# Kernel tuning notes

Hardware: AMD Instinct MI355X
Metric: run time of the kernel (lower is better)

Reference implementation:

```python
import jax, jax.numpy as jnp
import numpy as np

N_EMB = 768
N_HEAD = 12
B, T = 2, 2048
LN_EPS = 1e-5


def _ln(x, g, b):
    mu = jnp.mean(x, axis=-1, keepdims=True)
    var = jnp.mean((x - mu) ** 2, axis=-1, keepdims=True)
    return (x - mu) * jax.lax.rsqrt(var + LN_EPS) * g + b


def setup_inputs() -> dict:
    key = jax.random.key(0)
    ks = jax.random.split(key, 12)
    s = 0.02
    d = {
        "x": jax.random.normal(ks[0], (B, T, N_EMB), dtype=jnp.float32),
        "cond_len": 256,
        "padding_mask": jax.random.randint(ks[1], (B, T), 0, 2, dtype=jnp.int32),
        "g1": jnp.ones((N_EMB,), jnp.float32),
        "bln1": jnp.zeros((N_EMB,), jnp.float32),
        "g2": jnp.ones((N_EMB,), jnp.float32),
        "bln2": jnp.zeros((N_EMB,), jnp.float32),
        "Wq": jax.random.normal(ks[2], (N_EMB, N_EMB), jnp.float32) * s,
        "bq": jnp.zeros((N_EMB,), jnp.float32),
        "Wk": jax.random.normal(ks[3], (N_EMB, N_EMB), jnp.float32) * s,
        "bk": jnp.zeros((N_EMB,), jnp.float32),
        "Wv": jax.random.normal(ks[4], (N_EMB, N_EMB), jnp.float32) * s,
        "bv": jnp.zeros((N_EMB,), jnp.float32),
        "Wp": jax.random.normal(ks[5], (N_EMB, N_EMB), jnp.float32) * s,
        "bp": jnp.zeros((N_EMB,), jnp.float32),
        "W1": jax.random.normal(ks[6], (4 * N_EMB, N_EMB), jnp.float32) * s,
        "b1": jnp.zeros((4 * N_EMB,), jnp.float32),
        "W2": jax.random.normal(ks[7], (N_EMB, 4 * N_EMB), jnp.float32) * s,
        "b2": jnp.zeros((N_EMB,), jnp.float32),
    }
    return d


def reference(x, cond_len, padding_mask, g1, bln1, g2, bln2,
              Wq, bq, Wk, bk, Wv, bv, Wp, bp, W1, b1, W2, b2):
    Bc, Tc, C = x.shape
    H = N_HEAD
    Dh = C // H
    h = _ln(x, g1, bln1)
    q = (h @ Wq.T + bq).reshape(Bc, Tc, H, Dh)
    k = (h @ Wk.T + bk).reshape(Bc, Tc, H, Dh)
    v = (h @ Wv.T + bv).reshape(Bc, Tc, H, Dh)
    att = jnp.einsum("bqhd,bkhd->bhqk", q, k) * (1.0 / np.sqrt(Dh))
    # mask: key col allowed if col >= cond_len OR col < n_b, n_b = T - sum(pmask_b)
    n = Tc - jnp.sum(padding_mask, axis=1)  # [B]
    cols = jnp.arange(Tc)
    allowed = (cols[None, :] >= cond_len) | (cols[None, :] < n[:, None])  # [B,T]
    att = jnp.where(allowed[:, None, None, :], att, -jnp.inf)
    att = jax.nn.softmax(att, axis=-1)
    y = jnp.einsum("bhqk,bkhd->bqhd", att, v).reshape(Bc, Tc, C)
    x = x + (y @ Wp.T + bp)
    h2 = _ln(x, g2, bln2)
    m = jax.nn.gelu(h2 @ W1.T + b1, approximate=False) @ W2.T + b2
    return x + m
```

## Files before the change

kernel.cpp:

```cpp
#include <hip/hip_runtime.h>
#include <hip/hip_bf16.h>
#include <math.h>

typedef short bf16x8 __attribute__((ext_vector_type(8)));
typedef float f32x4 __attribute__((ext_vector_type(4)));
typedef float f32x16 __attribute__((ext_vector_type(16)));
typedef unsigned short us4 __attribute__((ext_vector_type(4)));

#define MFMA16(a, b, c) __builtin_amdgcn_mfma_f32_16x16x32_bf16(a, b, c, 0, 0, 0)
#define MFMA32(a, b, c) __builtin_amdgcn_mfma_f32_32x32x16_bf16(a, b, c, 0, 0, 0)

__device__ __forceinline__ unsigned short f2b(float f) {
  unsigned int u = __builtin_bit_cast(unsigned int, f);
  u += 0x7fffu + ((u >> 16) & 1u);
  return (unsigned short)(u >> 16);
}

__device__ __forceinline__ float b2f(unsigned short u) {
  unsigned int x = ((unsigned int)u) << 16;
  return __builtin_bit_cast(float, x);
}

__device__ __forceinline__ unsigned int cvtpk(float lo, float hiv) {
  unsigned int r;
  asm("v_cvt_pk_bf16_f32 %0, %1, %2" : "=v"(r) : "v"(lo), "v"(hiv));
  return r;
}

__device__ __forceinline__ void gload16(const void* g, void* l) {
  __builtin_amdgcn_global_load_lds((const unsigned int*)g, (unsigned int*)l, 16, 0, 0);
}

__global__ void cvt_qkv_k(const float* __restrict__ wq, const float* __restrict__ wk,
                          const float* __restrict__ wv, unsigned short* __restrict__ dst) {
  int i = blockIdx.x * 256 + threadIdx.x;
  if (i >= 2304 * 768 / 4) return;
  int e = i * 4;
  const float* src = e < 589824 ? wq + e : (e < 1179648 ? wk + (e - 589824) : wv + (e - 1179648));
  float4 v = *(const float4*)src;
  us4 o; o.x = f2b(v.x); o.y = f2b(v.y); o.z = f2b(v.z); o.w = f2b(v.w);
  ((us4*)dst)[i] = o;
}

__global__ void cvt3_k(const float* __restrict__ s0, const float* __restrict__ s1,
                       const float* __restrict__ s2, unsigned short* __restrict__ d0,
                       unsigned short* __restrict__ d1, unsigned short* __restrict__ d2) {
  const int n0 = 147456, n1 = 589824, n2 = 589824;
  int i = blockIdx.x * 256 + threadIdx.x;
  const float* s; unsigned short* d; int j = i;
  if (j < n0) { s = s0; d = d0; }
  else {
    j -= n0;
    if (j < n1) { s = s1; d = d1; }
    else { j -= n1; if (j >= n2) return; s = s2; d = d2; }
  }
  float4 v = ((const float4*)s)[j];
  us4 o; o.x = f2b(v.x); o.y = f2b(v.y); o.z = f2b(v.z); o.w = f2b(v.w);
  ((us4*)d)[j] = o;
}

__global__ void maskbias_k(const int* __restrict__ pm, const int* __restrict__ clp,
                           float* __restrict__ bias) {
  const int b = blockIdx.x, tid = threadIdx.x;
  int s = 0;
  for (int i = tid; i < 2048; i += 256) s += pm[b * 2048 + i];
  #pragma unroll
  for (int d = 1; d < 64; d <<= 1) s += __shfl_xor(s, d);
  __shared__ int red[4];
  if ((tid & 63) == 0) red[tid >> 6] = s;
  __syncthreads();
  const int n = 2048 - (red[0] + red[1] + red[2] + red[3]);
  const int cl = *clp;
  for (int t = tid; t < 2048; t += 256)
    bias[b * 2048 + t] = (t >= cl || t < n) ? 0.0f : -1e30f;
}

__global__ __launch_bounds__(256)
void ln_k(const float* __restrict__ x, const float* __restrict__ g,
          const float* __restrict__ be, unsigned short* __restrict__ out) {
  const int row = blockIdx.x * 4 + (threadIdx.x >> 6);
  const int l = threadIdx.x & 63;
  const float4* xr = (const float4*)(x + (size_t)row * 768);
  float4 v[3];
  float s = 0.f, s2 = 0.f;
  #pragma unroll
  for (int j = 0; j < 3; ++j) {
    v[j] = xr[l + j * 64];
    s += v[j].x + v[j].y + v[j].z + v[j].w;
    s2 += v[j].x * v[j].x + v[j].y * v[j].y + v[j].z * v[j].z + v[j].w * v[j].w;
  }
  #pragma unroll
  for (int d = 1; d < 64; d <<= 1) { s += __shfl_xor(s, d); s2 += __shfl_xor(s2, d); }
  const float mu = s * (1.0f / 768.0f);
  const float rstd = rsqrtf(s2 * (1.0f / 768.0f) - mu * mu + 1e-5f);
  #pragma unroll
  for (int j = 0; j < 3; ++j) {
    int c0 = (l + j * 64) * 4;
    us4 ov;
    ov.x = f2b((v[j].x - mu) * rstd * g[c0 + 0] + be[c0 + 0]);
    ov.y = f2b((v[j].y - mu) * rstd * g[c0 + 1] + be[c0 + 1]);
    ov.z = f2b((v[j].z - mu) * rstd * g[c0 + 2] + be[c0 + 2]);
    ov.w = f2b((v[j].w - mu) * rstd * g[c0 + 3] + be[c0 + 3]);
    *(us4*)(out + (size_t)row * 768 + c0) = ov;
  }
}

template<int MODE>
__global__ __launch_bounds__(256)
void gemm_k(const unsigned short* __restrict__ A, const unsigned short* __restrict__ W,
            const float* __restrict__ bias0, const float* __restrict__ bias1,
            const float* __restrict__ bias2, void* __restrict__ out,
            unsigned short* __restrict__ out2, int N, int K) {
  __shared__ __align__(16) unsigned short At[128 * 32];
  __shared__ __align__(16) unsigned short Wt[128 * 32];
  const int m0 = blockIdx.y * 128;
  const int n0 = blockIdx.x * 128;
  const int tid = threadIdx.x;
  const int w = tid >> 6, l = tid & 63;
  const int wm = w >> 1, wn = w & 1;
  const int lr = l & 15, lg = l >> 4;
  f32x4 acc[4][4] = {};

  const int nkt = K >> 5;
  for (int kt = 0; kt < nkt; ++kt) {
    const int k0 = kt << 5;
    #pragma unroll
    for (int i = 0; i < 2; ++i) {
      int slot = (i * 4 + w) * 64 + l;
      int row = slot >> 2, c8 = (slot & 3) << 3;
      gload16(A + (size_t)(m0 + row) * K + k0 + c8, (char*)At + ((i * 4 + w) * 64) * 16);
      gload16(W + (size_t)(n0 + row) * K + k0 + c8, (char*)Wt + ((i * 4 + w) * 64) * 16);
    }
    __syncthreads();
    bf16x8 af[4], bf[4];
    #pragma unroll
    for (int i = 0; i < 4; ++i) {
      af[i] = *(const bf16x8*)&At[(wm * 64 + i * 16 + lr) * 32 + lg * 8];
      bf[i] = *(const bf16x8*)&Wt[(wn * 64 + i * 16 + lr) * 32 + lg * 8];
    }
    #pragma unroll
    for (int mi = 0; mi < 4; ++mi)
      #pragma unroll
      for (int ni = 0; ni < 4; ++ni)
        acc[mi][ni] = MFMA16(af[mi], bf[ni], acc[mi][ni]);
    __syncthreads();
  }

  #pragma unroll
  for (int mi = 0; mi < 4; ++mi) {
    #pragma unroll
    for (int ni = 0; ni < 4; ++ni) {
      #pragma unroll
      for (int r = 0; r < 4; ++r) {
        int row = m0 + wm * 64 + mi * 16 + lg * 4 + r;
        int col = n0 + wn * 64 + ni * 16 + lr;
        float v = acc[mi][ni][r];
        if (MODE == 0) {
          float bb = col < 768 ? bias0[col] : (col < 1536 ? bias1[col - 768] : bias2[col - 1536]);
          v += bb;
          if (col < 1536) {
            ((unsigned short*)out)[(size_t)row * 2304 + col] = f2b(v);
          } else {
            int cc = col - 1536;
            int d = cc & 63, hh = cc >> 6;
            int b = row >> 11, t = row & 2047;
            out2[(((size_t)b * 12 + hh) * 64 + d) * 2048 + t] = f2b(v);
          }
        } else {
          v += bias0[col];
          v = 0.5f * v * (1.0f + erff(v * 0.70710678118f));
          ((unsigned short*)out)[(size_t)row * N + col] = f2b(v);
        }
      }
    }
  }
}

__global__ __launch_bounds__(256)
void gemm_pk(const unsigned short* __restrict__ A, const unsigned short* __restrict__ W,
             float* __restrict__ part, int N, int K, int KS) {
  __shared__ __align__(16) unsigned short At[128 * 32];
  __shared__ __align__(16) unsigned short Wt[128 * 32];
  const int m0 = blockIdx.y * 128;
  const int n0 = blockIdx.x * 128;
  const int kb = blockIdx.z * KS;
  const int tid = threadIdx.x;
  const int w = tid >> 6, l = tid & 63;
  const int wm = w >> 1, wn = w & 1;
  const int lr = l & 15, lg = l >> 4;
  f32x4 acc[4][4] = {};

  const int nkt = KS >> 5;
  for (int kt = 0; kt < nkt; ++kt) {
    const int k0 = kb + (kt << 5);
    #pragma unroll
    for (int i = 0; i < 2; ++i) {
      int slot = (i * 4 + w) * 64 + l;
      int row = slot >> 2, c8 = (slot & 3) << 3;
      gload16(A + (size_t)(m0 + row) * K + k0 + c8, (char*)At + ((i * 4 + w) * 64) * 16);
      gload16(W + (size_t)(n0 + row) * K + k0 + c8, (char*)Wt + ((i * 4 + w) * 64) * 16);
    }
    __syncthreads();
    bf16x8 af[4], bf[4];
    #pragma unroll
    for (int i = 0; i < 4; ++i) {
      af[i] = *(const bf16x8*)&At[(wm * 64 + i * 16 + lr) * 32 + lg * 8];
      bf[i] = *(const bf16x8*)&Wt[(wn * 64 + i * 16 + lr) * 32 + lg * 8];
    }
    #pragma unroll
    for (int mi = 0; mi < 4; ++mi)
      #pragma unroll
      for (int ni = 0; ni < 4; ++ni)
        acc[mi][ni] = MFMA16(af[mi], bf[ni], acc[mi][ni]);
    __syncthreads();
  }

  #pragma unroll
  for (int mi = 0; mi < 4; ++mi)
    #pragma unroll
    for (int ni = 0; ni < 4; ++ni)
      #pragma unroll
      for (int r = 0; r < 4; ++r) {
        int row = m0 + wm * 64 + mi * 16 + lg * 4 + r;
        int col = n0 + wn * 64 + ni * 16 + lr;
        part[((size_t)blockIdx.z * 4096 + row) * N + col] = acc[mi][ni][r];
      }
}

__global__ __launch_bounds__(512, 4)
void attn_k(const unsigned short* __restrict__ qkv, const unsigned short* __restrict__ vt,
            const float* __restrict__ abias, unsigned short* __restrict__ opart,
            float* __restrict__ mpart, float* __restrict__ lpart) {
  __shared__ __align__(16) unsigned short Kt[64 * 64];
  __shared__ __align__(16) unsigned short Vt[64 * 64];
  __shared__ __align__(16) float absh[512];
  const int d0 = blockIdx.x;
  const int c = d0 & 7, t_ = d0 >> 3;
  const int G = (t_ >> 3) * 8 + c;
  const int qt = t_ & 7;
  const int bh = G >> 2, split = G & 3;
  const int b = bh / 12, h = bh - b * 12;
  const int q0 = qt * 256;
  const int tb = split * 512;
  const int tid = threadIdx.x, w = tid >> 6, l = tid & 63;
  const int ql = l & 31, hi = l >> 5;
  const int q = q0 + w * 32 + ql;

  absh[tid] = abias[b * 2048 + tb + tid];

  bf16x8 qf[4];
  {
    const unsigned short* qrow = qkv + ((size_t)b * 2048 + q) * 2304 + h * 64 + hi * 8;
    #pragma unroll
    for (int ds = 0; ds < 4; ++ds) qf[ds] = *(const bf16x8*)(qrow + ds * 16);
  }

  f32x16 o0 = {}, o1 = {};
  float mrow = -1e30f, lrow = 0.f;

  const int srow = tid >> 3;
  const int scc = (tid & 7) ^ (srow & 7);
  const unsigned short* KgL = qkv + ((size_t)b * 2048 + tb + srow) * 2304 + 768 + h * 64 + scc * 8;
  const unsigned short* VgL = vt + ((size_t)bh * 64 + srow) * 2048 + tb + scc * 8;
  char* KtW = (char*)Kt + w * 1024;
  char* VtW = (char*)Vt + w * 1024;

  for (int tt = 0; tt < 8; ++tt) {
    gload16(KgL + (size_t)(tt * 64) * 2304, KtW);
    gload16(VgL + tt * 64, VtW);
    __syncthreads();

    f32x16 sa0 = {}, sa1 = {};
    {
      const int r0 = ql, r1 = 32 + ql;
      #pragma unroll
      for (int ds = 0; ds < 4; ++ds) {
        bf16x8 kf0 = *(const bf16x8*)((const char*)Kt + r0 * 128 + (((ds * 2 + hi) ^ (r0 & 7)) << 4));
        bf16x8 kf1 = *(const bf16x8*)((const char*)Kt + r1 * 128 + (((ds * 2 + hi) ^ (r1 & 7)) << 4));
        sa0 = MFMA32(kf0, qf[ds], sa0);
        sa1 = MFMA32(kf1, qf[ds], sa1);
      }
    }

    float mt = -1e30f;
    #pragma unroll
    for (int g = 0; g < 4; ++g) {
      float4 b0 = *(const float4*)&absh[tt * 64 + g * 8 + hi * 4];
      float4 b1 = *(const float4*)&absh[tt * 64 + 32 + g * 8 + hi * 4];
      float bb0[4] = {b0.x, b0.y, b0.z, b0.w};
      float bb1[4] = {b1.x, b1.y, b1.z, b1.w};
      #pragma unroll
      for (int r2 = 0; r2 < 4; ++r2) {
        float v0 = sa0[g * 4 + r2] * 0.125f + bb0[r2];
        float v1 = sa1[g * 4 + r2] * 0.125f + bb1[r2];
        sa0[g * 4 + r2] = v0; sa1[g * 4 + r2] = v1;
        mt = fmaxf(mt, fmaxf(v0, v1));
      }
    }
    mt = fmaxf(mt, __shfl_xor(mt, 32));

    const bool grow = mt > mrow;
    const float mnew = grow ? mt : mrow;
    const float corr = __expf(mrow - mnew);
    mrow = mnew;
    if (__any((int)grow)) {
      #pragma unroll
      for (int g = 0; g < 4; ++g)
        #pragma unroll
        for (int r2 = 0; r2 < 4; ++r2) {
          float cc2 = __shfl(corr, g * 8 + hi * 4 + r2);
          o0[g * 4 + r2] *= cc2;
          o1[g * 4 + r2] *= cc2;
        }
    }

    float rs = 0.f;
    auto half_pv = [&](const f32x16& sv, int ksb) {
      unsigned int u[8];
      #pragma unroll
      for (int g = 0; g < 4; ++g) {
        float e0 = __expf(sv[g * 4 + 0] - mnew);
        float e1 = __expf(sv[g * 4 + 1] - mnew);
        float e2 = __expf(sv[g * 4 + 2] - mnew);
        float e3 = __expf(sv[g * 4 + 3] - mnew);
        rs += (e0 + e1) + (e2 + e3);
        u[g * 2]     = cvtpk(e0, e1);
        u[g * 2 + 1] = cvtpk(e2, e3);
      }
      #pragma unroll
      for (int kh = 0; kh < 2; ++kh) {
        unsigned int a0 = u[kh * 4 + 0], a1 = u[kh * 4 + 1];
        unsigned int c0 = u[kh * 4 + 2], c1 = u[kh * 4 + 3];
        unsigned int xa0 = (unsigned int)__shfl_xor((int)a0, 32);
        unsigned int xa1 = (unsigned int)__shfl_xor((int)a1, 32);
        unsigned int xc0 = (unsigned int)__shfl_xor((int)c0, 32);
        unsigned int xc1 = (unsigned int)__shfl_xor((int)c1, 32);
        uint4 pk;
        pk.x = hi ? xc0 : a0;
        pk.y = hi ? xc1 : a1;
        pk.z = hi ? c0 : xa0;
        pk.w = hi ? c1 : xa1;
        bf16x8 pa = __builtin_bit_cast(bf16x8, pk);
        const int ks = ksb + kh;
        const int vr0 = ql, vr1 = 32 + ql;
        bf16x8 vf0 = *(const bf16x8*)((const char*)Vt + vr0 * 128 + (((ks * 2 + hi) ^ (vr0 & 7)) << 4));
        o0 = MFMA32(pa, vf0, o0);
        bf16x8 vf1 = *(const bf16x8*)((const char*)Vt + vr1 * 128 + (((ks * 2 + hi) ^ (vr1 & 7)) << 4));
        o1 = MFMA32(pa, vf1, o1);
      }
    };
    half_pv(sa0, 0);
    half_pv(sa1, 2);

    rs += __shfl_xor(rs, 32);
    lrow = lrow * corr + rs;
    __syncthreads();
  }

  const size_t orow0 = (size_t)split * 49152 + (size_t)bh * 2048 + q0 + w * 32;
  if (hi == 0) { mpart[orow0 + ql] = mrow; lpart[orow0 + ql] = lrow; }
  #pragma unroll
  for (int g = 0; g < 4; ++g)
    #pragma unroll
    for (int r2 = 0; r2 < 4; ++r2) {
      int oq = r2 + g * 8 + hi * 4;
      opart[(orow0 + oq) * 64 + ql]      = f2b(o0[g * 4 + r2]);
      opart[(orow0 + oq) * 64 + 32 + ql] = f2b(o1[g * 4 + r2]);
    }
}

__global__ __launch_bounds__(256)
void attn_comb_k(const unsigned short* __restrict__ op, const float* __restrict__ mp,
                 const float* __restrict__ lp, unsigned short* __restrict__ y) {
  const int row = blockIdx.x * 4 + (threadIdx.x >> 6);
  const int l = threadIdx.x & 63;
  float m0 = mp[row], m1 = mp[49152 + row], m2 = mp[2 * 49152 + row], m3 = mp[3 * 49152 + row];
  float M = fmaxf(fmaxf(m0, m1), fmaxf(m2, m3));
  float w0 = __expf(m0 - M), w1 = __expf(m1 - M), w2 = __expf(m2 - M), w3 = __expf(m3 - M);
  float den = w0 * lp[row] + w1 * lp[49152 + row] + w2 * lp[2 * 49152 + row] + w3 * lp[3 * 49152 + row];
  float num = w0 * b2f(op[((size_t)0 * 49152 + row) * 64 + l])
            + w1 * b2f(op[((size_t)1 * 49152 + row) * 64 + l])
            + w2 * b2f(op[((size_t)2 * 49152 + row) * 64 + l])
            + w3 * b2f(op[((size_t)3 * 49152 + row) * 64 + l]);
  const int bh = row >> 11, qq = row & 2047;
  const int bb = bh / 12, hh = bh - bb * 12;
  y[((size_t)(bb * 2048 + qq)) * 768 + hh * 64 + l] = f2b(num / den);
}

__global__ __launch_bounds__(256)
void proj_ln_k(const float* __restrict__ part, const float* __restrict__ bp,
               const float* __restrict__ xres, const float* __restrict__ g2,
               const float* __restrict__ bln2, float* __restrict__ xmid,
               unsigned short* __restrict__ h2) {
  const int row = blockIdx.x * 4 + (threadIdx.x >> 6);
  const int l = threadIdx.x & 63;
  float4 v[3];
  float s = 0.f, s2 = 0.f;
  #pragma unroll
  for (int j = 0; j < 3; ++j) {
    const int cc = l + j * 64;
    float4 a = ((const float4*)(xres + (size_t)row * 768))[cc];
    float4 bb = ((const float4*)bp)[cc];
    a.x += bb.x; a.y += bb.y; a.z += bb.z; a.w += bb.w;
    #pragma unroll
    for (int sp = 0; sp < 4; ++sp) {
      float4 pp = ((const float4*)(part + ((size_t)sp * 4096 + row) * 768))[cc];
      a.x += pp.x; a.y += pp.y; a.z += pp.z; a.w += pp.w;
    }
    v[j] = a;
    s += a.x + a.y + a.z + a.w;
    s2 += a.x * a.x + a.y * a.y + a.z * a.z + a.w * a.w;
  }
  #pragma unroll
  for (int d = 1; d < 64; d <<= 1) { s += __shfl_xor(s, d); s2 += __shfl_xor(s2, d); }
  const float mu = s * (1.0f / 768.0f);
  const float rstd = rsqrtf(s2 * (1.0f / 768.0f) - mu * mu + 1e-5f);
  #pragma unroll
  for (int j = 0; j < 3; ++j) {
    const int cc = l + j * 64;
    ((float4*)(xmid + (size_t)row * 768))[cc] = v[j];
    const int c0 = cc * 4;
    us4 ov;
    ov.x = f2b((v[j].x - mu) * rstd * g2[c0 + 0] + bln2[c0 + 0]);
    ov.y = f2b((v[j].y - mu) * rstd * g2[c0 + 1] + bln2[c0 + 1]);
    ov.z = f2b((v[j].z - mu) * rstd * g2[c0 + 2] + bln2[c0 + 2]);
    ov.w = f2b((v[j].w - mu) * rstd * g2[c0 + 3] + bln2[c0 + 3]);
    *(us4*)(h2 + (size_t)row * 768 + c0) = ov;
  }
}

__global__ void mlp2_comb_k(const float* __restrict__ part, const float* __restrict__ b2,
                            const float* __restrict__ xmid, float* __restrict__ out) {
  const int i = blockIdx.x * 256 + threadIdx.x;
  if (i >= 786432) return;
  const int c4 = i % 192;
  float4 a = ((const float4*)xmid)[i];
  float4 bb = ((const float4*)b2)[c4];
  a.x += bb.x; a.y += bb.y; a.z += bb.z; a.w += bb.w;
  #pragma unroll
  for (int sp = 0; sp < 4; ++sp) {
    float4 pp = ((const float4*)part)[(size_t)sp * 786432 + i];
    a.x += pp.x; a.y += pp.y; a.z += pp.z; a.w += pp.w;
  }
  ((float4*)out)[i] = a;
}

extern "C" void kernel_launch(void* const* d_in, const int* in_sizes, int n_in,
                              void* d_out, int out_size, void* d_ws, size_t ws_size,
                              hipStream_t stream) {
  const float* x    = (const float*)d_in[0];
  const int* condp  = (const int*)d_in[1];
  const int* pmask  = (const int*)d_in[2];
  const float* g1   = (const float*)d_in[3];
  const float* bln1 = (const float*)d_in[4];
  const float* g2   = (const float*)d_in[5];
  const float* bln2 = (const float*)d_in[6];
  const float* Wq   = (const float*)d_in[7];
  const float* bq   = (const float*)d_in[8];
  const float* Wk   = (const float*)d_in[9];
  const float* bk   = (const float*)d_in[10];
  const float* Wv   = (const float*)d_in[11];
  const float* bv   = (const float*)d_in[12];
  const float* Wp   = (const float*)d_in[13];
  const float* bp   = (const float*)d_in[14];
  const float* W1   = (const float*)d_in[15];
  const float* b1   = (const float*)d_in[16];
  const float* W2   = (const float*)d_in[17];
  const float* b2   = (const float*)d_in[18];

  char* p = (char*)d_ws;
  auto alloc = [&](size_t bytes) { char* r = p; p += (bytes + 255) & ~(size_t)255; return r; };
  unsigned short* Wqkv = (unsigned short*)alloc((size_t)2304 * 768 * 2);
  unsigned short* Wpb  = (unsigned short*)alloc((size_t)589824 * 2);
  unsigned short* W1b  = (unsigned short*)alloc((size_t)2359296 * 2);
  unsigned short* W2b  = (unsigned short*)alloc((size_t)2359296 * 2);
  unsigned short* hb   = (unsigned short*)alloc((size_t)4096 * 768 * 2);
  unsigned short* qkv  = (unsigned short*)alloc((size_t)4096 * 2304 * 2);
  unsigned short* vtb  = (unsigned short*)alloc((size_t)24 * 64 * 2048 * 2);
  float* xmid          = (float*)alloc((size_t)4096 * 768 * 4);
  unsigned short* h2b  = (unsigned short*)alloc((size_t)4096 * 768 * 2);
  float* abias         = (float*)alloc((size_t)2 * 2048 * 4);
  float* partial       = (float*)alloc((size_t)4 * 4096 * 768 * 4);
  unsigned short* yb   = hb;
  unsigned short* mlph = qkv;
  unsigned short* opart = (unsigned short*)partial;
  float* mpart = (float*)((char*)partial + (size_t)4 * 49152 * 64 * 2);
  float* lpart = mpart + 4 * 49152;

  cvt_qkv_k<<<1728, 256, 0, stream>>>(Wq, Wk, Wv, Wqkv);
  cvt3_k<<<5184, 256, 0, stream>>>(Wp, W1, W2, Wpb, W1b, W2b);
  maskbias_k<<<2, 256, 0, stream>>>(pmask, condp, abias);
  ln_k<<<1024, 256, 0, stream>>>(x, g1, bln1, hb);
  gemm_k<0><<<dim3(18, 32), 256, 0, stream>>>(hb, Wqkv, bq, bk, bv, qkv, vtb, 2304, 768);
  attn_k<<<768, 512, 0, stream>>>(qkv, vtb, abias, opart, mpart, lpart);
  attn_comb_k<<<12288, 256, 0, stream>>>(opart, mpart, lpart, yb);
  gemm_pk<<<dim3(6, 32, 4), 256, 0, stream>>>(yb, Wpb, partial, 768, 768, 192);
  proj_ln_k<<<1024, 256, 0, stream>>>(partial, bp, x, g2, bln2, xmid, h2b);
  gemm_k<2><<<dim3(24, 32), 256, 0, stream>>>(h2b, W1b, b1, nullptr, nullptr, mlph, nullptr, 3072, 768);
  gemm_pk<<<dim3(6, 32, 4), 256, 0, stream>>>(mlph, W2b, partial, 768, 3072, 768);
  mlp2_comb_k<<<3072, 256, 0, stream>>>(partial, b2, xmid, (float*)d_out);
}
```

Before: 348.9 us.

## Double-buffer GEMM tiles with BK=64, XOR-swizzled LDS, and XCD-aware block remap

Rewrites the GEMM and split-K GEMM main loops to double-buffer LDS tiles: the next 64-wide K slice is prefetched while MFMAs run on the current one, and each iteration needs one barrier instead of two. The LDS layout is XOR-swizzled by row to avoid bank conflicts when reading fragments. Launches become 1D, and block IDs are remapped so that blocks landing on the same XCD share M/N tiles for L2 reuse. In exchange LDS use rises fourfold to 64KB per block, which may lower occupancy.

Measured after the change: 343.6 us. No clear change (-1.5%).

```diff
diff --git a/kernel.cpp b/kernel.cpp
--- a/kernel.cpp
+++ b/kernel.cpp
@@ -105,44 +105,66 @@
   }
 }
 
+#define GEMM_STAGE(buf, k0)                                                        \
+  {                                                                                \
+    _Pragma("unroll")                                                              \
+    for (int i = 0; i < 4; ++i) {                                                  \
+      int slot = i * 256 + tid;                                                    \
+      int row = slot >> 3;                                                         \
+      int c = (slot & 7) ^ (row & 7);                                              \
+      gload16(A + (size_t)(m0 + row) * K + (k0) + c * 8,                           \
+              (char*)At[buf] + slot * 16);                                         \
+      gload16(W + (size_t)(n0 + row) * K + (k0) + c * 8,                           \
+              (char*)Wt[buf] + slot * 16);                                         \
+    }                                                                              \
+  }
+
+#define GEMM_COMPUTE(buf)                                                          \
+  {                                                                                \
+    const char* Ab = (const char*)At[buf];                                         \
+    const char* Wb = (const char*)Wt[buf];                                         \
+    _Pragma("unroll")                                                              \
+    for (int kk = 0; kk < 2; ++kk) {                                               \
+      bf16x8 af[4], bfr[4];                                                        \
+      _Pragma("unroll")                                                            \
+      for (int i = 0; i < 4; ++i) {                                                \
+        int ar = wm * 64 + i * 16 + lr;                                            \
+        af[i] = *(const bf16x8*)(Ab + ar * 128 + (((kk * 4 + lg) ^ (ar & 7)) << 4));\
+        int br = wn * 64 + i * 16 + lr;                                            \
+        bfr[i] = *(const bf16x8*)(Wb + br * 128 + (((kk * 4 + lg) ^ (br & 7)) << 4));\
+      }                                                                            \
+      _Pragma("unroll")                                                            \
+      for (int mi = 0; mi < 4; ++mi)                                               \
+        _Pragma("unroll")                                                          \
+        for (int ni = 0; ni < 4; ++ni)                                             \
+          acc[mi][ni] = MFMA16(af[mi], bfr[ni], acc[mi][ni]);                      \
+    }                                                                              \
+  }
+
 template<int MODE>
 __global__ __launch_bounds__(256)
 void gemm_k(const unsigned short* __restrict__ A, const unsigned short* __restrict__ W,
             const float* __restrict__ bias0, const float* __restrict__ bias1,
             const float* __restrict__ bias2, void* __restrict__ out,
-            unsigned short* __restrict__ out2, int N, int K) {
-  __shared__ __align__(16) unsigned short At[128 * 32];
-  __shared__ __align__(16) unsigned short Wt[128 * 32];
-  const int m0 = blockIdx.y * 128;
-  const int n0 = blockIdx.x * 128;
+            unsigned short* __restrict__ out2, int N, int K, int NN) {
+  __shared__ __align__(16) unsigned short At[2][128 * 64];
+  __shared__ __align__(16) unsigned short Wt[2][128 * 64];
+  const int nwg8 = gridDim.x >> 3;
+  const int swz = (blockIdx.x & 7) * nwg8 + (blockIdx.x >> 3);
+  const int m0 = (swz & 31) * 128;
+  const int n0 = ((swz >> 5) % NN) * 128;
   const int tid = threadIdx.x;
   const int w = tid >> 6, l = tid & 63;
   const int wm = w >> 1, wn = w & 1;
   const int lr = l & 15, lg = l >> 4;
   f32x4 acc[4][4] = {};
 
-  const int nkt = K >> 5;
+  const int nkt = K >> 6;
+  GEMM_STAGE(0, 0);
+  __syncthreads();
   for (int kt = 0; kt < nkt; ++kt) {
-    const int k0 = kt << 5;
-    #pragma unroll
-    for (int i = 0; i < 2; ++i) {
-      int slot = (i * 4 + w) * 64 + l;
-      int row = slot >> 2, c8 = (slot & 3) << 3;
-      gload16(A + (size_t)(m0 + row) * K + k0 + c8, (char*)At + ((i * 4 + w) * 64) * 16);
-      gload16(W + (size_t)(n0 + row) * K + k0 + c8, (char*)Wt + ((i * 4 + w) * 64) * 16);
-    }
-    __syncthreads();
-    bf16x8 af[4], bf[4];
-    #pragma unroll
-    for (int i = 0; i < 4; ++i) {
-      af[i] = *(const bf16x8*)&At[(wm * 64 + i * 16 + lr) * 32 + lg * 8];
-      bf[i] = *(const bf16x8*)&Wt[(wn * 64 + i * 16 + lr) * 32 + lg * 8];
-    }
-    #pragma unroll
-    for (int mi = 0; mi < 4; ++mi)
-      #pragma unroll
-      for (int ni = 0; ni < 4; ++ni)
-        acc[mi][ni] = MFMA16(af[mi], bf[ni], acc[mi][ni]);
+    if (kt + 1 < nkt) GEMM_STAGE((kt + 1) & 1, (kt + 1) << 6);
+    GEMM_COMPUTE(kt & 1);
     __syncthreads();
   }
 
@@ -178,40 +200,27 @@
 
 __global__ __launch_bounds__(256)
 void gemm_pk(const unsigned short* __restrict__ A, const unsigned short* __restrict__ W,
-             float* __restrict__ part, int N, int K, int KS) {
-  __shared__ __align__(16) unsigned short At[128 * 32];
-  __shared__ __align__(16) unsigned short Wt[128 * 32];
-  const int m0 = blockIdx.y * 128;
-  const int n0 = blockIdx.x * 128;
-  const int kb = blockIdx.z * KS;
+             float* __restrict__ part, int N, int K, int KS, int NN) {
+  __shared__ __align__(16) unsigned short At[2][128 * 64];
+  __shared__ __align__(16) unsigned short Wt[2][128 * 64];
+  const int nwg8 = gridDim.x >> 3;
+  const int swz = (blockIdx.x & 7) * nwg8 + (blockIdx.x >> 3);
+  const int m0 = (swz & 31) * 128;
+  const int rest = swz >> 5;
+  const int n0 = (rest % NN) * 128;
+  const int kb = (rest / NN) * KS;
   const int tid = threadIdx.x;
   const int w = tid >> 6, l = tid & 63;
   const int wm = w >> 1, wn = w & 1;
   const int lr = l & 15, lg = l >> 4;
   f32x4 acc[4][4] = {};
 
-  const int nkt = KS >> 5;
+  const int nkt = KS >> 6;
+  GEMM_STAGE(0, kb);
+  __syncthreads();
   for (int kt = 0; kt < nkt; ++kt) {
-    const int k0 = kb + (kt << 5);
-    #pragma unroll
-    for (int i = 0; i < 2; ++i) {
-      int slot = (i * 4 + w) * 64 + l;
-      int row = slot >> 2, c8 = (slot & 3) << 3;
-      gload16(A + (size_t)(m0 + row) * K + k0 + c8, (char*)At + ((i * 4 + w) * 64) * 16);
-      gload16(W + (size_t)(n0 + row) * K + k0 + c8, (char*)Wt + ((i * 4 + w) * 64) * 16);
-    }
-    __syncthreads();
-    bf16x8 af[4], bf[4];
-    #pragma unroll
-    for (int i = 0; i < 4; ++i) {
-      af[i] = *(const bf16x8*)&At[(wm * 64 + i * 16 + lr) * 32 + lg * 8];
-      bf[i] = *(const bf16x8*)&Wt[(wn * 64 + i * 16 + lr) * 32 + lg * 8];
-    }
-    #pragma unroll
-    for (int mi = 0; mi < 4; ++mi)
-      #pragma unroll
-      for (int ni = 0; ni < 4; ++ni)
-        acc[mi][ni] = MFMA16(af[mi], bf[ni], acc[mi][ni]);
+    if (kt + 1 < nkt) GEMM_STAGE((kt + 1) & 1, kb + ((kt + 1) << 6));
+    GEMM_COMPUTE(kt & 1);
     __syncthreads();
   }
 
@@ -223,7 +232,7 @@
       for (int r = 0; r < 4; ++r) {
         int row = m0 + wm * 64 + mi * 16 + lg * 4 + r;
         int col = n0 + wn * 64 + ni * 16 + lr;
-        part[((size_t)blockIdx.z * 4096 + row) * N + col] = acc[mi][ni][r];
+        part[((size_t)(rest / NN) * 4096 + row) * N + col] = acc[mi][ni][r];
       }
 }
 
@@ -491,12 +500,12 @@
   cvt3_k<<<5184, 256, 0, stream>>>(Wp, W1, W2, Wpb, W1b, W2b);
   maskbias_k<<<2, 256, 0, stream>>>(pmask, condp, abias);
   ln_k<<<1024, 256, 0, stream>>>(x, g1, bln1, hb);
-  gemm_k<0><<<dim3(18, 32), 256, 0, stream>>>(hb, Wqkv, bq, bk, bv, qkv, vtb, 2304, 768);
+  gemm_k<0><<<576, 256, 0, stream>>>(hb, Wqkv, bq, bk, bv, qkv, vtb, 2304, 768, 18);
   attn_k<<<768, 512, 0, stream>>>(qkv, vtb, abias, opart, mpart, lpart);
   attn_comb_k<<<12288, 256, 0, stream>>>(opart, mpart, lpart, yb);
-  gemm_pk<<<dim3(6, 32, 4), 256, 0, stream>>>(yb, Wpb, partial, 768, 768, 192);
+  gemm_pk<<<768, 256, 0, stream>>>(yb, Wpb, partial, 768, 768, 192, 6);
   proj_ln_k<<<1024, 256, 0, stream>>>(partial, bp, x, g2, bln2, xmid, h2b);
-  gemm_k<2><<<dim3(24, 32), 256, 0, stream>>>(h2b, W1b, b1, nullptr, nullptr, mlph, nullptr, 3072, 768);
-  gemm_pk<<<dim3(6, 32, 4), 256, 0, stream>>>(mlph, W2b, partial, 768, 3072, 768);
+  gemm_k<2><<<768, 256, 0, stream>>>(h2b, W1b, b1, nullptr, nullptr, mlph, nullptr, 3072, 768, 24);
+  gemm_pk<<<768, 256, 0, stream>>>(mlph, W2b, partial, 768, 3072, 768, 6);
   mlp2_comb_k<<<3072, 256, 0, stream>>>(partial, b2, xmid, (float*)d_out);
 }
```
